# Kernel optimization log

Hardware: AMD Instinct MI355X
Metric: run time of the kernel (lower is better)

## Reference

```python
import jax, jax.numpy as jnp
import numpy as np

D = 512
HEADS, DIM_HEAD, LANDMARKS, PINV_ITERS = 8, 64, 256, 6
CONV_K = 33  # residual depthwise conv kernel over sequence dim


def _ln(x, g, b, eps=1e-5):
    mu = x.mean(-1, keepdims=True)
    var = ((x - mu) ** 2).mean(-1, keepdims=True)
    return (x - mu) / jnp.sqrt(var + eps) * g + b


def _moe(x, gw, gb, f1w, f1b, l1g, l1b, f2w, f2b, l2g, l2b, k):
    # Dense grouped-expert evaluation (same math as per-token dispatch in torch source).
    scores = x @ gw + gb                               # [B,N,E]
    topk_s, topk_i = jax.lax.top_k(scores, k)          # [B,N,k]
    h = jnp.einsum('bnd,edh->benh', x, f1w) + f1b[None, :, None, :]
    h = jax.nn.relu(_ln(h, l1g[None, :, None, :], l1b[None, :, None, :]))
    o = jnp.einsum('benh,ehd->bend', h, f2w) + f2b[None, :, None, :]
    o = _ln(o, l2g[None, :, None, :], l2b[None, :, None, :])  # [B,E,N,D]
    o = jnp.take_along_axis(jnp.swapaxes(o, 1, 2), topk_i[..., None], axis=2)  # [B,N,k,D]
    w = jax.nn.softmax(topk_s, axis=-1)[..., None]
    return (w * o).sum(axis=2) + x


def _pinv(x, iters):
    # Moore-Penrose iterative pseudoinverse (lucidrains nystrom-attention)
    col = jnp.abs(x).sum(-1).max()
    row = jnp.abs(x).sum(-2).max()
    z = jnp.swapaxes(x, -1, -2) / (col * row)
    I = jnp.eye(x.shape[-1], dtype=x.dtype)
    for _ in range(iters):
        xz = x @ z
        z = 0.25 * z @ (13 * I - xz @ (15 * I - xz @ (7 * I - xz)))
    return z


def _nystrom(x, qkv_w, out_w, out_b, conv_w):
    b, n, _ = x.shape
    m, h, dh = LANDMARKS, HEADS, DIM_HEAD
    pad = (m - n % m) % m
    x = jnp.pad(x, ((0, 0), (pad, 0), (0, 0)))  # pad at FRONT, as in source
    npd = n + pad
    qkv = x @ qkv_w                              # [b, npd, 3*h*dh]
    q, k, v = [t.reshape(b, npd, h, dh).transpose(0, 2, 1, 3) for t in jnp.split(qkv, 3, axis=-1)]
    q = q * dh ** -0.5
    l = npd // m
    q_l = q.reshape(b, h, m, l, dh).mean(3)      # landmark means
    k_l = k.reshape(b, h, m, l, dh).mean(3)
    attn1 = jax.nn.softmax(jnp.einsum('bhid,bhjd->bhij', q, k_l), -1)    # [b,h,npd,m]
    attn2 = jax.nn.softmax(jnp.einsum('bhid,bhjd->bhij', q_l, k_l), -1)  # [b,h,m,m]
    attn3 = jax.nn.softmax(jnp.einsum('bhid,bhjd->bhij', q_l, k), -1)    # [b,h,m,npd]
    out = (attn1 @ _pinv(attn2, PINV_ITERS)) @ (attn3 @ v)               # [b,h,npd,dh]
    res = jax.lax.conv_general_dilated(
        v, conv_w, (1, 1), [(CONV_K // 2, CONV_K // 2), (0, 0)],
        dimension_numbers=('NCHW', 'OIHW', 'NCHW'), feature_group_count=h)
    out = out + res
    out = out.transpose(0, 2, 1, 3).reshape(b, npd, h * dh)
    out = out @ out_w + out_b
    return out[:, -n:]


def setup_inputs() -> dict:
    key = jax.random.key(0)
    ks = iter(jax.random.split(key, 64))
    def rn(shape, s=0.02):
        return jax.random.normal(next(ks), shape, jnp.float32) * s
    inp = {'features': jax.random.normal(next(ks), (4, 6000, D), jnp.float32)}
    inp['cls_token'] = rn((1, 1, D), 1e-6)
    def moe_params(pfx, E):
        inp[pfx + '_gate_w'] = rn((D, E)); inp[pfx + '_gate_b'] = jnp.zeros((E,), jnp.float32)
        inp[pfx + '_fc1_w'] = rn((E, D, D)); inp[pfx + '_fc1_b'] = jnp.zeros((E, D), jnp.float32)
        inp[pfx + '_ln1_g'] = jnp.ones((E, D), jnp.float32); inp[pfx + '_ln1_b'] = jnp.zeros((E, D), jnp.float32)
        inp[pfx + '_fc2_w'] = rn((E, D, D)); inp[pfx + '_fc2_b'] = jnp.zeros((E, D), jnp.float32)
        inp[pfx + '_ln2_g'] = jnp.ones((E, D), jnp.float32); inp[pfx + '_ln2_b'] = jnp.zeros((E, D), jnp.float32)
    moe_params('moe1', 2)
    moe_params('moe2', 4)
    def layer_params(pfx):
        inp[pfx + '_norm_g'] = jnp.ones((D,), jnp.float32); inp[pfx + '_norm_b'] = jnp.zeros((D,), jnp.float32)
        inp[pfx + '_qkv_w'] = rn((D, 3 * HEADS * DIM_HEAD))
        inp[pfx + '_out_w'] = rn((HEADS * DIM_HEAD, D)); inp[pfx + '_out_b'] = jnp.zeros((D,), jnp.float32)
        inp[pfx + '_conv_w'] = rn((HEADS, 1, CONV_K, 1))
    layer_params('l1')
    layer_params('l2')
    return inp


def reference(features, cls_token,
              moe1_gate_w, moe1_gate_b, moe1_fc1_w, moe1_fc1_b, moe1_ln1_g, moe1_ln1_b, moe1_fc2_w, moe1_fc2_b, moe1_ln2_g, moe1_ln2_b,
              moe2_gate_w, moe2_gate_b, moe2_fc1_w, moe2_fc1_b, moe2_ln1_g, moe2_ln1_b, moe2_fc2_w, moe2_fc2_b, moe2_ln2_g, moe2_ln2_b,
              l1_norm_g, l1_norm_b, l1_qkv_w, l1_out_w, l1_out_b, l1_conv_w,
              l2_norm_g, l2_norm_b, l2_qkv_w, l2_out_w, l2_out_b, l2_conv_w):
    B, N, _ = features.shape
    _H = int(np.ceil(np.sqrt(N)))
    add = _H * _H - N
    h = jnp.concatenate([features, features[:, :add]], axis=1)      # square pad by wrap
    h = jnp.concatenate([jnp.broadcast_to(cls_token, (B, 1, D)), h], axis=1)
    h = _moe(h, moe1_gate_w, moe1_gate_b, moe1_fc1_w, moe1_fc1_b, moe1_ln1_g, moe1_ln1_b, moe1_fc2_w, moe1_fc2_b, moe1_ln2_g, moe1_ln2_b, k=1)
    h = h + _nystrom(_ln(h, l1_norm_g, l1_norm_b), l1_qkv_w, l1_out_w, l1_out_b, l1_conv_w)
    h = _moe(h, moe2_gate_w, moe2_gate_b, moe2_fc1_w, moe2_fc1_b, moe2_ln1_g, moe2_ln1_b, moe2_fc2_w, moe2_fc2_b, moe2_ln2_g, moe2_ln2_b, k=2)
    h = h + _nystrom(_ln(h, l2_norm_g, l2_norm_b), l2_qkv_w, l2_out_w, l2_out_b, l2_conv_w)
    return (h[:, 0], h[:, 1:])
```

## Files before the change

kernel.cpp:

```cpp
#include <hip/hip_runtime.h>
#include <hip/hip_bf16.h>

constexpr int BATCH = 4;
constexpr int NTOK  = 6085;
constexpr int BN_TOK = BATCH * NTOK;
constexpr int NPD   = 6144;
constexpr int RPAD  = BATCH * NPD;
constexpr int DMODEL = 512;
constexpr int NH = 8, DH = 64;
constexpr int NBH = BATCH * NH;
constexpr int LGRP = NPD / 256;
constexpr int PAD_FRONT = 59;
constexpr int CONVK = 33;
constexpr int NCH = 4;

typedef __attribute__((ext_vector_type(8))) short short8v;
typedef __attribute__((ext_vector_type(4))) float f32x4;

__device__ __forceinline__ unsigned short f2bf(float f) {
  unsigned u = __float_as_uint(f);
  u += 0x7FFF + ((u >> 16) & 1);
  return (unsigned short)(u >> 16);
}
__device__ __forceinline__ float bf2f(unsigned short h) {
  return __uint_as_float((unsigned)h << 16);
}


__global__ void k_build_h(const float* __restrict__ feat, const float* __restrict__ cls,
                          float* __restrict__ H) {
  size_t total = (size_t)BN_TOK * DMODEL;
  for (size_t idx = (size_t)blockIdx.x * blockDim.x + threadIdx.x; idx < total;
       idx += (size_t)gridDim.x * blockDim.x) {
    int d = (int)(idx & 511);
    size_t tok = idx >> 9;
    int b = (int)(tok / NTOK), n = (int)(tok % NTOK);
    float v;
    if (n == 0) v = cls[d];
    else {
      int i = n - 1; if (i >= 6000) i -= 6000;
      v = feat[((size_t)b * 6000 + i) * DMODEL + d];
    }
    H[idx] = v;
  }
}

__global__ void k_diag_fill(float* __restrict__ out, size_t n, float val) {
  for (size_t i = (size_t)blockIdx.x * blockDim.x + threadIdx.x; i < n;
       i += (size_t)gridDim.x * blockDim.x)
    out[i] = val;
}

__global__ __launch_bounds__(256) void k_wconv(const float* __restrict__ W, int ldb,
    unsigned short* __restrict__ hi, unsigned short* __restrict__ lo) {
  __shared__ unsigned short Th[64][80], Tl[64][80];
  int bk = blockIdx.y * 64, bn = blockIdx.x * 64;
  int t = threadIdx.x;
  int kr = t >> 2, cq = (t & 3) * 16;
  const float* src = W + (size_t)(bk + kr) * ldb + bn + cq;
  #pragma unroll
  for (int q = 0; q < 4; ++q) {
    float4 v = *(const float4*)(src + q * 4);
    float vs[4] = {v.x, v.y, v.z, v.w};
    #pragma unroll
    for (int e = 0; e < 4; ++e) {
      int n = cq + q * 4 + e;
      unsigned short h = f2bf(vs[e]);
      Th[n][kr] = h;
      Tl[n][kr] = f2bf(vs[e] - bf2f(h));
    }
  }
  __syncthreads();
  int nr = t >> 2, kq = (t & 3) * 16;
  size_t o = (size_t)(bn + nr) * 512 + bk + kq;
  *(short8v*)&hi[o]     = *(const short8v*)&Th[nr][kq];
  *(short8v*)&hi[o + 8] = *(const short8v*)&Th[nr][kq + 8];
  *(short8v*)&lo[o]     = *(const short8v*)&Tl[nr][kq];
  *(short8v*)&lo[o + 8] = *(const short8v*)&Tl[nr][kq + 8];
}

__global__ __launch_bounds__(256) void k_gemm_mfma(const float* __restrict__ A,
    const unsigned short* __restrict__ BtH, const unsigned short* __restrict__ BtL,
    const float* __restrict__ bias, float* __restrict__ C,
    int M, int lda, int ldc, float alpha, int omode)
{
  __shared__ unsigned short AsH[128][40], AsL[128][40];
  __shared__ unsigned short BsH[128][40], BsL[128][40];
  int bm = blockIdx.y * 128, bn = blockIdx.x * 128;
  int tid = threadIdx.x;
  int wave = tid >> 6, lane = tid & 63;
  int mo = (wave >> 1) * 64, no = (wave & 1) * 64;
  int r16 = lane & 15, g = lane >> 4;
  f32x4 acc[4][4] = {};
  int srow = tid >> 1, shalf = (tid & 1) * 16;
  const float* aptr = A + (size_t)(bm + srow) * lda + shalf;
  bool avalid = (bm + srow) < M;
  const unsigned short* bhptr = BtH + (size_t)(bn + srow) * 512 + shalf;
  const unsigned short* blptr = BtL + (size_t)(bn + srow) * 512 + shalf;
  for (int k0 = 0; k0 < 512; k0 += 32) {
    unsigned short h8[16], l8[16];
    #pragma unroll
    for (int q = 0; q < 4; ++q) {
      float4 v = avalid ? *(const float4*)(aptr + k0 + q * 4) : make_float4(0.f, 0.f, 0.f, 0.f);
      float vs[4] = {v.x, v.y, v.z, v.w};
      #pragma unroll
      for (int e = 0; e < 4; ++e) {
        unsigned short hh = f2bf(vs[e]);
        h8[q * 4 + e] = hh;
        l8[q * 4 + e] = f2bf(vs[e] - bf2f(hh));
      }
    }
    *(short8v*)&AsH[srow][shalf]     = *(short8v*)&h8[0];
    *(short8v*)&AsH[srow][shalf + 8] = *(short8v*)&h8[8];
    *(short8v*)&AsL[srow][shalf]     = *(short8v*)&l8[0];
    *(short8v*)&AsL[srow][shalf + 8] = *(short8v*)&l8[8];
    *(short8v*)&BsH[srow][shalf]     = *(const short8v*)(bhptr + k0);
    *(short8v*)&BsH[srow][shalf + 8] = *(const short8v*)(bhptr + k0 + 8);
    *(short8v*)&BsL[srow][shalf]     = *(const short8v*)(blptr + k0);
    *(short8v*)&BsL[srow][shalf + 8] = *(const short8v*)(blptr + k0 + 8);
    __syncthreads();
    short8v ah[4], al[4], bh[4], bl[4];
    #pragma unroll
    for (int mt = 0; mt < 4; ++mt) {
      ah[mt] = *(const short8v*)&AsH[mo + mt * 16 + r16][g * 8];
      al[mt] = *(const short8v*)&AsL[mo + mt * 16 + r16][g * 8];
    }
    #pragma unroll
    for (int nt = 0; nt < 4; ++nt) {
      bh[nt] = *(const short8v*)&BsH[no + nt * 16 + r16][g * 8];
      bl[nt] = *(const short8v*)&BsL[no + nt * 16 + r16][g * 8];
    }
    #pragma unroll
    for (int mt = 0; mt < 4; ++mt)
      #pragma unroll
      for (int nt = 0; nt < 4; ++nt) {
        acc[mt][nt] = __builtin_amdgcn_mfma_f32_16x16x32_bf16(ah[mt], bh[nt], acc[mt][nt], 0, 0, 0);
        acc[mt][nt] = __builtin_amdgcn_mfma_f32_16x16x32_bf16(ah[mt], bl[nt], acc[mt][nt], 0, 0, 0);
        acc[mt][nt] = __builtin_amdgcn_mfma_f32_16x16x32_bf16(al[mt], bh[nt], acc[mt][nt], 0, 0, 0);
      }
    __syncthreads();
  }
  #pragma unroll
  for (int mt = 0; mt < 4; ++mt)
    #pragma unroll
    for (int nt = 0; nt < 4; ++nt)
      #pragma unroll
      for (int j = 0; j < 4; ++j) {
        int gr = bm + mo + mt * 16 + g * 4 + j;
        int gc = bn + no + nt * 16 + r16;
        if (gr >= M) continue;
        float v = alpha * acc[mt][nt][j] + (bias ? bias[gc] : 0.f);
        if (omode == 0) {
          C[(size_t)gr * ldc + gc] = v;
        } else if (omode == 2) {
          int bb = gr / NPD, ii = gr % NPD;
          if (ii >= PAD_FRONT)
            C[((size_t)bb * NTOK + ii - PAD_FRONT) * 512 + gc] += v;
        } else {
          int bb = gr / NPD, ii = gr % NPD;
          int hh = gc >> 6, dd = gc & 63;
          C[(((size_t)bb * NH + hh) * NPD + ii) * 64 + dd] = v;
        }
      }
}

__global__ __launch_bounds__(256) void k_gemm_mfma2(const float* __restrict__ A,
    const float* __restrict__ Bt, float* __restrict__ C,
    float alpha, int omode, float cdiag, int premap)
{
  __shared__ unsigned short AsH[128][40], AsL[128][40];
  __shared__ unsigned short BsH[128][40], BsL[128][40];
  size_t zo = (size_t)blockIdx.z * 65536;
  int bm = blockIdx.y * 128, bn = blockIdx.x * 128;
  int tid = threadIdx.x;
  int wave = tid >> 6, lane = tid & 63;
  int mo = (wave >> 1) * 64, no = (wave & 1) * 64;
  int r16 = lane & 15, g = lane >> 4;
  f32x4 acc[4][4] = {};
  int srow = tid >> 1, shalf = (tid & 1) * 16;
  int grow = bm + srow;
  int gn = bn + srow;
  for (int k0 = 0; k0 < 256; k0 += 32) {
    unsigned short h8[16], l8[16];
    #pragma unroll
    for (int q = 0; q < 4; ++q) {
      float4 v = *(const float4*)&A[zo + (size_t)grow * 256 + k0 + shalf + q * 4];
      float vs[4] = {v.x, v.y, v.z, v.w};
      #pragma unroll
      for (int e = 0; e < 4; ++e) {
        float a = vs[e];
        if (premap) a = ((grow == (k0 + shalf + q * 4 + e)) ? 7.f : 0.f) - a;
        unsigned short hh = f2bf(a);
        h8[q * 4 + e] = hh;
        l8[q * 4 + e] = f2bf(a - bf2f(hh));
      }
    }
    *(short8v*)&AsH[srow][shalf]     = *(short8v*)&h8[0];
    *(short8v*)&AsH[srow][shalf + 8] = *(short8v*)&h8[8];
    *(short8v*)&AsL[srow][shalf]     = *(short8v*)&l8[0];
    *(short8v*)&AsL[srow][shalf + 8] = *(short8v*)&l8[8];
    #pragma unroll
    for (int q = 0; q < 4; ++q) {
      float4 v = *(const float4*)&Bt[zo + (size_t)gn * 256 + k0 + shalf + q * 4];
      float vs[4] = {v.x, v.y, v.z, v.w};
      #pragma unroll
      for (int e = 0; e < 4; ++e) {
        unsigned short hh = f2bf(vs[e]);
        h8[q * 4 + e] = hh;
        l8[q * 4 + e] = f2bf(vs[e] - bf2f(hh));
      }
    }
    *(short8v*)&BsH[srow][shalf]     = *(short8v*)&h8[0];
    *(short8v*)&BsH[srow][shalf + 8] = *(short8v*)&h8[8];
    *(short8v*)&BsL[srow][shalf]     = *(short8v*)&l8[0];
    *(short8v*)&BsL[srow][shalf + 8] = *(short8v*)&l8[8];
    __syncthreads();
    short8v ah[4], al[4], bh[4], bl[4];
    #pragma unroll
    for (int mt = 0; mt < 4; ++mt) {
      ah[mt] = *(const short8v*)&AsH[mo + mt * 16 + r16][g * 8];
      al[mt] = *(const short8v*)&AsL[mo + mt * 16 + r16][g * 8];
    }
    #pragma unroll
    for (int nt = 0; nt < 4; ++nt) {
      bh[nt] = *(const short8v*)&BsH[no + nt * 16 + r16][g * 8];
      bl[nt] = *(const short8v*)&BsL[no + nt * 16 + r16][g * 8];
    }
    #pragma unroll
    for (int mt = 0; mt < 4; ++mt)
      #pragma unroll
      for (int nt = 0; nt < 4; ++nt) {
        acc[mt][nt] = __builtin_amdgcn_mfma_f32_16x16x32_bf16(ah[mt], bh[nt], acc[mt][nt], 0, 0, 0);
        acc[mt][nt] = __builtin_amdgcn_mfma_f32_16x16x32_bf16(ah[mt], bl[nt], acc[mt][nt], 0, 0, 0);
        acc[mt][nt] = __builtin_amdgcn_mfma_f32_16x16x32_bf16(al[mt], bh[nt], acc[mt][nt], 0, 0, 0);
      }
    __syncthreads();
  }
  #pragma unroll
  for (int mt = 0; mt < 4; ++mt)
    #pragma unroll
    for (int nt = 0; nt < 4; ++nt)
      #pragma unroll
      for (int j = 0; j < 4; ++j) {
        int gr = bm + mo + mt * 16 + g * 4 + j;
        int gc = bn + no + nt * 16 + r16;
        float v;
        if (omode == 5) v = ((gr == gc) ? cdiag : 0.f) - acc[mt][nt][j];
        else            v = alpha * acc[mt][nt][j];
        C[zo + (size_t)gr * 256 + gc] = v;
      }
}

__global__ __launch_bounds__(256) void k_tpose(const float* __restrict__ in,
                                               float* __restrict__ out) {
  __shared__ float Ts[64][65];
  int bx = blockIdx.x * 64, by = blockIdx.y * 64;
  size_t zo = (size_t)blockIdx.z * 65536;
  int t = threadIdx.x;
  int r = t >> 4, c4 = (t & 15) * 4;
  #pragma unroll
  for (int u = 0; u < 4; ++u) {
    float4 v = *(const float4*)&in[zo + (size_t)(by + r + u * 16) * 256 + bx + c4];
    Ts[r + u * 16][c4 + 0] = v.x; Ts[r + u * 16][c4 + 1] = v.y;
    Ts[r + u * 16][c4 + 2] = v.z; Ts[r + u * 16][c4 + 3] = v.w;
  }
  __syncthreads();
  #pragma unroll
  for (int u = 0; u < 4; ++u) {
    int rr = r + u * 16;
    float4 v = make_float4(Ts[c4][rr], Ts[c4 + 1][rr], Ts[c4 + 2][rr], Ts[c4 + 3][rr]);
    *(float4*)&out[zo + (size_t)(bx + rr) * 256 + by + c4] = v;
  }
}

__global__ void k_y0(const float* __restrict__ A2, float* __restrict__ Y,
                     const unsigned int* __restrict__ sc) {
  float scale = 1.f / (__uint_as_float(sc[0]) * __uint_as_float(sc[1]));
  size_t total = (size_t)NBH * 65536;
  for (size_t idx = (size_t)blockIdx.x * blockDim.x + threadIdx.x; idx < total;
       idx += (size_t)gridDim.x * blockDim.x)
    Y[idx] = A2[idx] * scale;
}

__global__ __launch_bounds__(256) void k_gemm(const float* __restrict__ A,
    const float* __restrict__ B,
    const float* __restrict__ bias, float* __restrict__ C,
    int M, int N, int K, int lda, int ldb, int ldc,
    long long sA, long long sB, long long sC, float alpha, int omode, float cdiag)
{
  __shared__ float As[16][65];
  __shared__ float Bs[16][65];
  int z = blockIdx.z;
  A += (size_t)z * (size_t)sA;
  B += (size_t)z * (size_t)sB;
  int bm = blockIdx.y * 64, bn = blockIdx.x * 64;
  int tid = threadIdx.x;
  int tr = tid >> 4, tc = tid & 15;
  int ar = tid >> 2, aq = tid & 3;
  int br = tid >> 4, bq = tid & 15;
  float acc[4][4] = {};
  for (int k0 = 0; k0 < K; k0 += 16) {
    {
      int gr = bm + ar;
      float4 v = make_float4(0.f, 0.f, 0.f, 0.f);
      if (gr < M) v = *(const float4*)&A[(size_t)gr * lda + k0 + aq * 4];
      As[aq * 4 + 0][ar] = v.x; As[aq * 4 + 1][ar] = v.y;
      As[aq * 4 + 2][ar] = v.z; As[aq * 4 + 3][ar] = v.w;
    }
    {
      float4 v = *(const float4*)&B[(size_t)(k0 + br) * ldb + bn + bq * 4];
      Bs[br][bq * 4 + 0] = v.x; Bs[br][bq * 4 + 1] = v.y;
      Bs[br][bq * 4 + 2] = v.z; Bs[br][bq * 4 + 3] = v.w;
    }
    __syncthreads();
    #pragma unroll
    for (int kk = 0; kk < 16; ++kk) {
      float a[4], bv[4];
      #pragma unroll
      for (int i = 0; i < 4; ++i) a[i] = As[kk][tr * 4 + i];
      #pragma unroll
      for (int j = 0; j < 4; ++j) bv[j] = Bs[kk][tc * 4 + j];
      #pragma unroll
      for (int i = 0; i < 4; ++i)
        #pragma unroll
        for (int j = 0; j < 4; ++j) acc[i][j] += a[i] * bv[j];
    }
    __syncthreads();
  }
  #pragma unroll
  for (int i = 0; i < 4; ++i) {
    int gr = bm + tr * 4 + i;
    if (gr >= M) continue;
    #pragma unroll
    for (int j = 0; j < 4; ++j) {
      int gc = bn + tc * 4 + j;
      float v;
      if (omode == 5) {
        v = ((gr == gc) ? cdiag : 0.f) - acc[i][j];
      } else {
        v = alpha * acc[i][j] + (bias ? bias[gc] : 0.f);
      }
      C[(size_t)z * (size_t)sC + (size_t)gr * ldc + gc] = v;
    }
  }
}

__global__ void k_gate(const float* __restrict__ X, const float* __restrict__ gw,
                       const float* __restrict__ gb, float* __restrict__ WT, int E, int k) {
  int tok = blockIdx.x; int lane = threadIdx.x;
  const float* x = X + (size_t)tok * DMODEL;
  float s[4] = {0.f, 0.f, 0.f, 0.f};
  for (int d = lane; d < DMODEL; d += 64) {
    float xv = x[d];
    for (int e = 0; e < E; ++e) s[e] += xv * gw[(size_t)d * E + e];
  }
  #pragma unroll
  for (int off = 32; off; off >>= 1) {
    #pragma unroll
    for (int e = 0; e < 4; ++e) s[e] += __shfl_down(s[e], off);
  }
  if (lane == 0) {
    for (int e = 0; e < E; ++e) s[e] += gb[e];
    float w[4] = {0.f, 0.f, 0.f, 0.f};
    int i1 = 0;
// ... 48 lines not shown
  float* h = H + (size_t)row * 512;
  #pragma unroll
  for (int j = 0; j < 8; ++j) {
    int d = lane + 64 * j;
    h[d] += w * ((x[d] - mu) * rstd * g[d] + b[d]);
  }
}

__global__ void k_ln_pad(const float* __restrict__ H, float* __restrict__ XLn,
                         const float* __restrict__ g, const float* __restrict__ b) {
  int row = blockIdx.x; int lane = threadIdx.x;
  int bb = row / NPD, i = row % NPD;
  float* y = XLn + (size_t)row * 512;
  if (i < PAD_FRONT) {
    #pragma unroll
    for (int j = 0; j < 8; ++j) y[lane + 64 * j] = 0.f;
    return;
  }
  const float* x = H + ((size_t)bb * NTOK + (i - PAD_FRONT)) * 512;
  float mu, rstd; wave_ln_stats(x, lane, mu, rstd);
  #pragma unroll
  for (int j = 0; j < 8; ++j) {
    int d = lane + 64 * j;
    y[d] = (x[d] - mu) * rstd * g[d] + b[d];
  }
}

__global__ void k_xmean(const float* __restrict__ XLn, float* __restrict__ Xm) {
  int z = blockIdx.x;
  int c = threadIdx.x;
  int b = z >> 8, jm = z & 255;
  const float* base = XLn + ((size_t)b * NPD + jm * LGRP) * 512 + c;
  float s = 0.f;
  #pragma unroll
  for (int t = 0; t < LGRP; ++t) s += base[(size_t)t * 512];
  Xm[(size_t)z * 512 + c] = s * (1.f / LGRP);
}

__global__ __launch_bounds__(256) void k_attn2(const float* __restrict__ QL,
                                               const float* __restrict__ KL,
                                               float* __restrict__ A2) {
  int z = blockIdx.x; int bh = z >> 8, j = z & 255;
  int b = bh >> 3, h = bh & 7;
  int t = threadIdx.x;
  __shared__ float q[64]; __shared__ float red[256];
  __shared__ float mshare, sshare;
  if (t < 64) q[t] = QL[((size_t)b * 256 + j) * 512 + h * 64 + t];
  __syncthreads();
  const float* kl = KL + ((size_t)b * 256 + t) * 512 + h * 64;
  float s = 0.f;
  #pragma unroll
  for (int d = 0; d < 64; ++d) s += q[d] * kl[d];
  red[t] = s; __syncthreads();
  for (int st = 128; st; st >>= 1) { if (t < st) red[t] = fmaxf(red[t], red[t + st]); __syncthreads(); }
  if (t == 0) mshare = red[0];
  __syncthreads();
  float e = expf(s - mshare);
  red[t] = e; __syncthreads();
  for (int st = 128; st; st >>= 1) { if (t < st) red[t] += red[t + st]; __syncthreads(); }
  if (t == 0) sshare = red[0];
  __syncthreads();
  A2[((size_t)bh * 256 + j) * 256 + t] = e / sshare;
}

__global__ __launch_bounds__(256) void k_pinv_scalars(const float* __restrict__ A2,
                                                      unsigned int* __restrict__ sc) {
  int bh = blockIdx.x; int t = threadIdx.x;
  const float* A = A2 + (size_t)bh * 65536;
  float rowsum = 0.f, colsum = 0.f;
  for (int jj = 0; jj < 256; ++jj) {
    rowsum += fabsf(A[(size_t)t * 256 + jj]);
    colsum += fabsf(A[(size_t)jj * 256 + t]);
  }
  __shared__ float sh[256];
  sh[t] = rowsum; __syncthreads();
  for (int s = 128; s; s >>= 1) { if (t < s) sh[t] = fmaxf(sh[t], sh[t + s]); __syncthreads(); }
  if (t == 0) atomicMax(&sc[0], __float_as_uint(sh[0]));
  __syncthreads();
  sh[t] = colsum; __syncthreads();
  for (int s = 128; s; s >>= 1) { if (t < s) sh[t] = fmaxf(sh[t], sh[t + s]); __syncthreads(); }
  if (t == 0) atomicMax(&sc[1], __float_as_uint(sh[0]));
}

__global__ void k_zinit(const float* __restrict__ A2, float* __restrict__ Z,
                        const unsigned int* __restrict__ sc) {
  float scale = 1.f / (__uint_as_float(sc[0]) * __uint_as_float(sc[1]));
  size_t total = (size_t)NBH * 65536;
  for (size_t idx = (size_t)blockIdx.x * blockDim.x + threadIdx.x; idx < total;
       idx += (size_t)gridDim.x * blockDim.x) {
    size_t bh = idx >> 16; int r = (int)((idx >> 8) & 255); int cc = (int)(idx & 255);
    Z[idx] = A2[(bh << 16) + (size_t)cc * 256 + r] * scale;
  }
}

__global__ __launch_bounds__(256) void k_flash_mfma(
    const float* __restrict__ Qp, long long Qsb, long long Qsh, int Qsr,
    const float* __restrict__ Kp, long long Ksb, long long Ksh, int Ksr,
    const float* __restrict__ Vp, long long Vsb, long long Vsh, int Vsr,
    float* __restrict__ Op, long long Osb, long long Osh, int Osr,
    float* __restrict__ Opart, float* __restrict__ ML,
    int tiles_per_chunk, int mode)
{
  int jt = blockIdx.x, bh = blockIdx.y, ch = blockIdx.z;
  int b = bh >> 3, h = bh & 7;
  const float* Qb = Qp + (size_t)b * Qsb + (size_t)h * Qsh;
  const float* Kb = Kp + (size_t)b * Ksb + (size_t)h * Ksh;
  const float* Vb = Vp + (size_t)b * Vsb + (size_t)h * Vsh;
  int tid = threadIdx.x;
  int wave = tid >> 6, lane = tid & 63;
  int r16 = lane & 15, g = lane >> 4;
  int q0 = jt * 64 + wave * 16;

  __shared__ unsigned short KsH[64][72], KsL[64][72];
  __shared__ unsigned short VtH[64][72], VtL[64][72];

  short8v qh[2], ql[2];
  #pragma unroll
  for (int kk = 0; kk < 2; ++kk) {
    const float* qr = Qb + (size_t)(q0 + r16) * Qsr + kk * 32 + g * 8;
    float4 v0 = *(const float4*)qr;
    float4 v1 = *(const float4*)(qr + 4);
    float vs[8] = {v0.x, v0.y, v0.z, v0.w, v1.x, v1.y, v1.z, v1.w};
    unsigned short hh[8], llo[8];
    #pragma unroll
    for (int e = 0; e < 8; ++e) {
      hh[e] = f2bf(vs[e]); llo[e] = f2bf(vs[e] - bf2f(hh[e]));
    }
    qh[kk] = *(short8v*)&hh[0];
    ql[kk] = *(short8v*)&llo[0];
  }

  f32x4 O4[4] = {};
  float m[4], lsum[4];
  #pragma unroll
  for (int j = 0; j < 4; ++j) { m[j] = -1e30f; lsum[j] = 0.f; }

  int skey = tid >> 2, sq = (tid & 3) * 16;
  int t0 = ch * tiles_per_chunk;
  for (int tt = t0; tt < t0 + tiles_per_chunk; ++tt) {
    int key0 = tt * 64;
    __syncthreads();
    {
      const float* krow = Kb + (size_t)(key0 + skey) * Ksr + sq;
      const float* vrow = Vb + (size_t)(key0 + skey) * Vsr + sq;
      #pragma unroll
      for (int q = 0; q < 4; ++q) {
        float4 kv = *(const float4*)(krow + q * 4);
        float4 vv = *(const float4*)(vrow + q * 4);
        float ks[4] = {kv.x, kv.y, kv.z, kv.w};
        float vvs[4] = {vv.x, vv.y, vv.z, vv.w};
        #pragma unroll
        for (int e = 0; e < 4; ++e) {
          int d = sq + q * 4 + e;
          unsigned short khh = f2bf(ks[e]);
          KsH[skey][d] = khh;
          KsL[skey][d] = f2bf(ks[e] - bf2f(khh));
          unsigned short vhh = f2bf(vvs[e]);
          VtH[d][skey] = vhh;
          VtL[d][skey] = f2bf(vvs[e] - bf2f(vhh));
        }
      }
    }
    __syncthreads();
    f32x4 S[4] = {};
    #pragma unroll
    for (int kk = 0; kk < 2; ++kk)
      #pragma unroll
      for (int nt = 0; nt < 4; ++nt) {
        short8v kh = *(const short8v*)&KsH[nt * 16 + r16][kk * 32 + g * 8];
        short8v kl = *(const short8v*)&KsL[nt * 16 + r16][kk * 32 + g * 8];
        S[nt] = __builtin_amdgcn_mfma_f32_16x16x32_bf16(qh[kk], kh, S[nt], 0, 0, 0);
        S[nt] = __builtin_amdgcn_mfma_f32_16x16x32_bf16(qh[kk], kl, S[nt], 0, 0, 0);
        S[nt] = __builtin_amdgcn_mfma_f32_16x16x32_bf16(ql[kk], kh, S[nt], 0, 0, 0);
      }
    float tmax[4];
    #pragma unroll
    for (int j = 0; j < 4; ++j)
      tmax[j] = fmaxf(fmaxf(S[0][j], S[1][j]), fmaxf(S[2][j], S[3][j]));
    #pragma unroll
    for (int off = 8; off; off >>= 1)
      #pragma unroll
      for (int j = 0; j < 4; ++j) tmax[j] = fmaxf(tmax[j], __shfl_xor(tmax[j], off));
    float corr[4];
    #pragma unroll
    for (int j = 0; j < 4; ++j) {
      float mn = fmaxf(m[j], tmax[j]);
      corr[j] = expf(m[j] - mn);
      m[j] = mn;
    }
    __syncthreads();
    float tl[4] = {0.f, 0.f, 0.f, 0.f};
    #pragma unroll
    for (int nt = 0; nt < 4; ++nt)
      #pragma unroll
      for (int j = 0; j < 4; ++j) {
        float p = expf(S[nt][j] - m[j]);
        tl[j] += p;
        unsigned short ph = f2bf(p);
        KsH[wave * 16 + g * 4 + j][nt * 16 + r16] = ph;
        KsL[wave * 16 + g * 4 + j][nt * 16 + r16] = f2bf(p - bf2f(ph));
      }
    #pragma unroll
    for (int off = 8; off; off >>= 1)
      #pragma unroll
      for (int j = 0; j < 4; ++j) tl[j] += __shfl_xor(tl[j], off);
    #pragma unroll
    for (int j = 0; j < 4; ++j) lsum[j] = lsum[j] * corr[j] + tl[j];
    #pragma unroll
    for (int nt = 0; nt < 4; ++nt)
      #pragma unroll
      for (int j = 0; j < 4; ++j) O4[nt][j] *= corr[j];
    #pragma unroll
    for (int kk = 0; kk < 2; ++kk) {
      short8v ph = *(const short8v*)&KsH[wave * 16 + r16][kk * 32 + g * 8];
      short8v pl = *(const short8v*)&KsL[wave * 16 + r16][kk * 32 + g * 8];
      #pragma unroll
      for (int nt = 0; nt < 4; ++nt) {
        short8v vh = *(const short8v*)&VtH[nt * 16 + r16][kk * 32 + g * 8];
        short8v vl = *(const short8v*)&VtL[nt * 16 + r16][kk * 32 + g * 8];
        O4[nt] = __builtin_amdgcn_mfma_f32_16x16x32_bf16(ph, vh, O4[nt], 0, 0, 0);
        O4[nt] = __builtin_amdgcn_mfma_f32_16x16x32_bf16(ph, vl, O4[nt], 0, 0, 0);
        O4[nt] = __builtin_amdgcn_mfma_f32_16x16x32_bf16(pl, vh, O4[nt], 0, 0, 0);
      }
    }
  }
  if (mode == 0) {
    float* Ob = Op + (size_t)b * Osb + (size_t)h * Osh;
    float inv[4];
    #pragma unroll
    for (int j = 0; j < 4; ++j) inv[j] = 1.f / lsum[j];
    #pragma unroll
    for (int nt = 0; nt < 4; ++nt)
      #pragma unroll
      for (int j = 0; j < 4; ++j)
        Ob[(size_t)(q0 + g * 4 + j) * Osr + nt * 16 + r16] = O4[nt][j] * inv[j];
  } else {
    #pragma unroll
    for (int j = 0; j < 4; ++j) {
      size_t rowbase = ((size_t)ch * NBH + bh) * 256 + q0 + g * 4 + j;
      #pragma unroll
      for (int nt = 0; nt < 4; ++nt)
        Opart[rowbase * 64 + nt * 16 + r16] = O4[nt][j];
      if (r16 == 0) { ML[rowbase * 2] = m[j]; ML[rowbase * 2 + 1] = lsum[j]; }
    }
  }
}

__global__ __launch_bounds__(256) void k_flash_comb(const float* __restrict__ Opart,
                                                    const float* __restrict__ ML,
                                                    float* __restrict__ A3V) {
  int jt = blockIdx.x, bh = blockIdx.y;
  int t = threadIdx.x;
  int jr = t >> 4, q16 = t & 15;
  int row = jt * 16 + jr;
  float mv[NCH], lv[NCH];
  float M = -1e30f;
  #pragma unroll
  for (int ch = 0; ch < NCH; ++ch) {
    size_t base = (((size_t)ch * NBH + bh) * 256 + row);
    mv[ch] = ML[base * 2]; lv[ch] = ML[base * 2 + 1];
    M = fmaxf(M, mv[ch]);
  }
  float L = 0.f;
  float4 O = make_float4(0.f, 0.f, 0.f, 0.f);
  #pragma unroll
  for (int ch = 0; ch < NCH; ++ch) {
    float c = expf(mv[ch] - M);
    L += c * lv[ch];
    size_t base = (((size_t)ch * NBH + bh) * 256 + row);
    float4 o = *(const float4*)&Opart[base * 64 + q16 * 4];
    O.x += c * o.x; O.y += c * o.y; O.z += c * o.z; O.w += c * o.w;
  }
  float inv = 1.f / L;
  *(float4*)&A3V[((size_t)bh * 256 + row) * 64 + q16 * 4] =
      make_float4(O.x * inv, O.y * inv, O.z * inv, O.w * inv);
}

__global__ __launch_bounds__(256) void k_conv_add(const float* __restrict__ Vp,
                                                  const float* __restrict__ cw,
                                                  float* __restrict__ out) {
  int it = blockIdx.x, bh = blockIdx.y;
  int b = bh >> 3, h = bh & 7;
  int i0 = it * 128;
  int t = threadIdx.x;
  __shared__ float Vs[160][64];
  const float* vb = Vp + (size_t)bh * NPD * 64;
  #pragma unroll
  for (int u = 0; u < 10; ++u) {
    int idx = t + 256 * u;
    int r = idx >> 4, c4 = (idx & 15) * 4;
    int gi = i0 - 16 + r;
    float4 v = make_float4(0.f, 0.f, 0.f, 0.f);
    if (gi >= 0 && gi < NPD) v = *(const float4*)&vb[(size_t)gi * 64 + c4];
    *(float4*)&Vs[r][c4] = v;
  }
  __syncthreads();
  float w[CONVK];
  #pragma unroll
  for (int p = 0; p < CONVK; ++p) w[p] = cw[h * CONVK + p];
  int wave = t >> 6, d = t & 63;
  for (int rr = wave * 32; rr < wave * 32 + 32; ++rr) {
    float acc = 0.f;
    #pragma unroll
    for (int p = 0; p < CONVK; ++p) acc += w[p] * Vs[rr + p][d];
    out[((size_t)b * NPD + i0 + rr) * 512 + h * 64 + d] += acc;
  }
}

__global__ void k_out_write(const float* __restrict__ H, float* __restrict__ out) {
  size_t n0 = (size_t)BATCH * 512;
  size_t total = n0 + (size_t)BATCH * (NTOK - 1) * 512;
  for (size_t idx = (size_t)blockIdx.x * blockDim.x + threadIdx.x; idx < total;
       idx += (size_t)gridDim.x * blockDim.x) {
    float v;
    if (idx < n0) {
      int b = (int)(idx >> 9); int d = (int)(idx & 511);
      v = H[((size_t)b * NTOK) * 512 + d];
    } else {
      size_t r = idx - n0;
      size_t bj = r >> 9; int d = (int)(r & 511);
      int b = (int)(bj / (NTOK - 1)); int j = (int)(bj % (NTOK - 1));
      v = H[((size_t)b * NTOK + 1 + j) * 512 + d];
    }
    out[idx] = v;
  }
}


extern "C" void kernel_launch(void* const* d_in, const int* in_sizes, int n_in,
                              void* d_out, int out_size, void* d_ws, size_t ws_size,
                              hipStream_t stream) {
  (void)in_sizes; (void)n_in;

  const float* feat = (const float*)d_in[0];
  const float* cls  = (const float*)d_in[1];
  const float* m1_gw = (const float*)d_in[2];  const float* m1_gb = (const float*)d_in[3];
  const float* m1_f1w = (const float*)d_in[4]; const float* m1_f1b = (const float*)d_in[5];
  const float* m1_l1g = (const float*)d_in[6]; const float* m1_l1b = (const float*)d_in[7];
  const float* m1_f2w = (const float*)d_in[8]; const float* m1_f2b = (const float*)d_in[9];
  const float* m1_l2g = (const float*)d_in[10]; const float* m1_l2b = (const float*)d_in[11];
  const float* m2_gw = (const float*)d_in[12]; const float* m2_gb = (const float*)d_in[13];
  const float* m2_f1w = (const float*)d_in[14]; const float* m2_f1b = (const float*)d_in[15];
  const float* m2_l1g = (const float*)d_in[16]; const float* m2_l1b = (const float*)d_in[17];
  const float* m2_f2w = (const float*)d_in[18]; const float* m2_f2b = (const float*)d_in[19];
  const float* m2_l2g = (const float*)d_in[20]; const float* m2_l2b = (const float*)d_in[21];
  const float* l1_ng = (const float*)d_in[22]; const float* l1_nb = (const float*)d_in[23];
  const float* l1_qkvw = (const float*)d_in[24]; const float* l1_outw = (const float*)d_in[25];
  const float* l1_outb = (const float*)d_in[26]; const float* l1_convw = (const float*)d_in[27];
  const float* l2_ng = (const float*)d_in[28]; const float* l2_nb = (const float*)d_in[29];
  const float* l2_qkvw = (const float*)d_in[30]; const float* l2_outw = (const float*)d_in[31];
  const float* l2_outb = (const float*)d_in[32]; const float* l2_convw = (const float*)d_in[33];

  constexpr size_t SZ_H    = (size_t)BN_TOK * 512;
  constexpr size_t SZ_ROW  = (size_t)RPAD * 512;
  float* W = (float*)d_ws;
  float* H  = W;
  float* WT = W + SZ_H;
  unsigned int* SC = (unsigned int*)(W + SZ_H + 97360);
  float* pool = W + SZ_H + 97360 + 16;

  float* R2 = pool;
  float* R3 = pool + SZ_ROW;
  float* R4 = pool + 2 * SZ_ROW;
  float* SMALL = pool + 3 * SZ_ROW;
  float* Xm  = SMALL;
  float* QL  = SMALL + 524288;
  float* KL  = SMALL + 1048576;
  float* A2  = SMALL + 1572864;
  float* Zb  = SMALL + 3670016;
  float* XZ  = SMALL + 5767168;
  float* Wa  = SMALL + 7864320;
  float* Wb  = SMALL + 9961472;
  float* A3V = SMALL + 12058624;
  float* W2b = SMALL + 12582912;
  size_t total_f = (SZ_H + 97360 + 16) + 3 * SZ_ROW + 13107200;
  if (total_f * 4 > ws_size) {
    k_diag_fill<<<2048, 256, 0, stream>>>((float*)d_out, (size_t)out_size,
                                          (float)(ws_size >> 20));
    return;
  }

  k_build_h<<<2048, 256, 0, stream>>>(feat, cls, H);

  auto run_moe = [&](const float* gw, const float* gb, const float* f1w, const float* f1b,
                     const float* l1g, const float* l1b, const float* f2w, const float* f2b,
                     const float* l2g, const float* l2b, int E, int k) {
    float* T1 = R2; float* T2 = R3; float* Xsnap = R4;
    unsigned short* BtHi = (unsigned short*)A2;
    unsigned short* BtLo = (unsigned short*)(A2 + 131072);
    hipMemcpyAsync(Xsnap, H, SZ_H * 4, hipMemcpyDeviceToDevice, stream);
    k_gate<<<BN_TOK, 64, 0, stream>>>(H, gw, gb, WT, E, k);
    dim3 g(4, (BN_TOK + 127) / 128, 1);
    for (int e = 0; e < E; ++e) {
      k_wconv<<<dim3(8, 8), 256, 0, stream>>>(f1w + (size_t)e * 262144, 512, BtHi, BtLo);
      k_gemm_mfma<<<g, 256, 0, stream>>>(Xsnap, BtHi, BtLo, f1b + e * 512, T1,
          BN_TOK, 512, 512, 1.f, 0);
      k_ln_relu<<<BN_TOK, 64, 0, stream>>>(T1, l1g + e * 512, l1b + e * 512);
      k_wconv<<<dim3(8, 8), 256, 0, stream>>>(f2w + (size_t)e * 262144, 512, BtHi, BtLo);
      k_gemm_mfma<<<g, 256, 0, stream>>>(T1, BtHi, BtLo, f2b + e * 512, T2,
          BN_TOK, 512, 512, 1.f, 0);
      k_ln_waccum<<<BN_TOK, 64, 0, stream>>>(T2, H, l2g + e * 512, l2b + e * 512, WT, e);
    }
  };

  auto run_attn = [&](const float* ng, const float* nb, const float* qkvw, const float* outw,
                      const float* outb, const float* convw) {
    float* XLn = R2; float* AttnO = R2;
    float* Kp = R3; float* Qb = R3; float* Vp = R4;
    k_ln_pad<<<RPAD, 64, 0, stream>>>(H, XLn, ng, nb);
    k_xmean<<<BATCH * 256, 512, 0, stream>>>(XLn, Xm);
    k_gemm<<<dim3(8, 16, 1), 256, 0, stream>>>(Xm, qkvw, nullptr, QL,
        1024, 512, 512, 512, 1536, 512, 0, 0, 0, 0.125f, 0, 0.f);
    k_gemm<<<dim3(8, 16, 1), 256, 0, stream>>>(Xm, qkvw + 512, nullptr, KL,
        1024, 512, 512, 512, 1536, 512, 0, 0, 0, 1.f, 0, 0.f);
    k_attn2<<<NBH * 256, 256, 0, stream>>>(QL, KL, A2);
    hipMemsetAsync(SC, 0, 8, stream);
    k_pinv_scalars<<<NBH, 256, 0, stream>>>(A2, SC);
    k_y0<<<2048, 256, 0, stream>>>(A2, Zb, SC);
    k_zinit<<<2048, 256, 0, stream>>>(A2, Wb, SC);
    float* Y = Zb; float* Z = Wb; float* F1 = XZ; float* F2 = Wa;
    dim3 gq(2, 2, NBH);
    for (int it = 0; it < 6; ++it) {
      k_gemm_mfma2<<<gq, 256, 0, stream>>>(Y, A2, F1, 1.f, 0, 0.f, 0);
      k_gemm_mfma2<<<gq, 256, 0, stream>>>(A2, Y, F2, 1.f, 0, 0.f, 0);
      k_gemm_mfma2<<<gq, 256, 0, stream>>>(F1, F2, Y, 1.f, 5, 15.f, 1);
      k_gemm_mfma2<<<gq, 256, 0, stream>>>(Y, F2, F1, 1.f, 5, 13.f, 0);
      k_gemm_mfma2<<<gq, 256, 0, stream>>>(Z, F1, F2, 0.25f, 0, 0.f, 0);
      float* tz = Z; Z = F2; F2 = tz;
      if (it < 5)
        k_tpose<<<dim3(4, 4, NBH), 256, 0, stream>>>(Z, Y);
    }
    unsigned short* BtQH = (unsigned short*)Wa;
    unsigned short* BtQL = (unsigned short*)(Wa + 393216);
    k_wconv<<<dim3(24, 8), 256, 0, stream>>>(qkvw, 1536, BtQH, BtQL);
    dim3 gr(4, (RPAD + 127) / 128, 1);
    k_gemm_mfma<<<gr, 256, 0, stream>>>(XLn, BtQH + 512 * 512, BtQL + 512 * 512, nullptr,
        Kp, RPAD, 512, 512, 1.f, 3);
    k_gemm_mfma<<<gr, 256, 0, stream>>>(XLn, BtQH + 1024 * 512, BtQL + 1024 * 512, nullptr,
        Vp, RPAD, 512, 512, 1.f, 3);
    k_flash_mfma<<<dim3(4, NBH, NCH), 256, 0, stream>>>(
        QL, 131072LL, 64LL, 512,
        Kp, (long long)NH * NPD * 64, (long long)NPD * 64, 64,
        Vp, (long long)NH * NPD * 64, (long long)NPD * 64, 64,
        nullptr, 0, 0, 0, XZ, Xm, NPD / (64 * NCH), 1);
    k_flash_comb<<<dim3(16, NBH), 256, 0, stream>>>(XZ, Xm, A3V);
    k_gemm<<<dim3(1, 4, NBH), 256, 0, stream>>>(Z, A3V, nullptr, W2b,
        256, 64, 256, 256, 64, 64, 65536, 16384, 16384, 1.f, 0, 0.f);
    k_gemm_mfma<<<gr, 256, 0, stream>>>(XLn, BtQH, BtQL, nullptr,
        Qb, RPAD, 512, 512, 0.125f, 0);
    k_flash_mfma<<<dim3(NPD / 64, NBH, 1), 256, 0, stream>>>(
        Qb, (long long)NPD * 512, 64LL, 512,
        KL, 131072LL, 64LL, 512,
        W2b, 131072LL, 16384LL, 64,
        AttnO, (long long)NPD * 512, 64LL, 512,
        nullptr, nullptr, 256 / 64, 0);
    k_conv_add<<<dim3(NPD / 128, NBH), 256, 0, stream>>>(Vp, convw, AttnO);
    unsigned short* BtOH = (unsigned short*)Wa;
    unsigned short* BtOL = (unsigned short*)(Wa + 131072);
    k_wconv<<<dim3(8, 8), 256, 0, stream>>>(outw, 512, BtOH, BtOL);
    k_gemm_mfma<<<gr, 256, 0, stream>>>(AttnO, BtOH, BtOL, outb,
        H, RPAD, 512, 512, 1.f, 2);
  };

  run_moe(m1_gw, m1_gb, m1_f1w, m1_f1b, m1_l1g, m1_l1b, m1_f2w, m1_f2b, m1_l2g, m1_l2b, 2, 1);
  run_attn(l1_ng, l1_nb, l1_qkvw, l1_outw, l1_outb, l1_convw);
  run_moe(m2_gw, m2_gb, m2_f1w, m2_f1b, m2_l1g, m2_l1b, m2_f2w, m2_f2b, m2_l2g, m2_l2b, 4, 2);
  run_attn(l2_ng, l2_nb, l2_qkvw, l2_outw, l2_outb, l2_convw);

  k_out_write<<<2048, 256, 0, stream>>>(H, (float*)d_out);
}
```

Before: 3.734 ms.

## Pre-split K/V into bf16 hi/lo, pretransposed V, drop one pinv GEMM, more flash chunks

K and V projections now emit bf16 hi/lo pairs directly from the GEMM epilogue, and V is pre-transposed so the flash kernel loads tiles with vector copies instead of converting fp32 per tile. The landmark K and W2 are pre-converted likewise. The pinv loop replaces the Y·A2 GEMM with a transpose of A2·Y, exploiting symmetry of the iteration. The flash chunk count is doubled for more parallelism, and conv_add reads from the transposed bf16 V. These changes add extra conversion and transpose passes and shift precision to hi/lo bf16 reconstruction.

After: 3.611 ms. 1.03x faster.

```diff
diff --git a/kernel.cpp b/kernel.cpp
--- a/kernel.cpp
+++ b/kernel.cpp
@@ -12,7 +12,7 @@
 constexpr int LGRP = NPD / 256;
 constexpr int PAD_FRONT = 59;
 constexpr int CONVK = 33;
-constexpr int NCH = 4;
+constexpr int NCH = 8;
 
 typedef __attribute__((ext_vector_type(8))) short short8v;
 typedef __attribute__((ext_vector_type(4))) float f32x4;
@@ -82,7 +82,7 @@
 __global__ __launch_bounds__(256) void k_gemm_mfma(const float* __restrict__ A,
     const unsigned short* __restrict__ BtH, const unsigned short* __restrict__ BtL,
     const float* __restrict__ bias, float* __restrict__ C,
-    int M, int lda, int ldc, float alpha, int omode)
+    int M, int lda, int ldc, float alpha, int omode, unsigned short* __restrict__ Clo)
 {
   __shared__ unsigned short AsH[128][40], AsL[128][40];
   __shared__ unsigned short BsH[128][40], BsL[128][40];
@@ -156,10 +156,17 @@
           int bb = gr / NPD, ii = gr % NPD;
           if (ii >= PAD_FRONT)
             C[((size_t)bb * NTOK + ii - PAD_FRONT) * 512 + gc] += v;
+        } else if (omode == 3) {
+          int bb = gr / NPD, ii = gr % NPD;
+          int hh = gc >> 6, dd = gc & 63;
+          C[(((size_t)bb * NH + hh) * NPD + ii) * 64 + dd] = v;
         } else {
           int bb = gr / NPD, ii = gr % NPD;
           int hh = gc >> 6, dd = gc & 63;
-          C[(((size_t)bb * NH + hh) * NPD + ii) * 64 + dd] = v;
+          size_t idx = (((size_t)bb * NH + hh) * NPD + ii) * 64 + dd;
+          unsigned short hi = f2bf(v);
+          ((unsigned short*)C)[idx] = hi;
+          Clo[idx] = f2bf(v - bf2f(hi));
         }
       }
 }
@@ -280,6 +287,17 @@
   for (size_t idx = (size_t)blockIdx.x * blockDim.x + threadIdx.x; idx < total;
        idx += (size_t)gridDim.x * blockDim.x)
     Y[idx] = A2[idx] * scale;
+}
+
+__global__ void k_zinit(const float* __restrict__ A2, float* __restrict__ Z,
+                        const unsigned int* __restrict__ sc) {
+  float scale = 1.f / (__uint_as_float(sc[0]) * __uint_as_float(sc[1]));
+  size_t total = (size_t)NBH * 65536;
+  for (size_t idx = (size_t)blockIdx.x * blockDim.x + threadIdx.x; idx < total;
+       idx += (size_t)gridDim.x * blockDim.x) {
+    size_t bh = idx >> 16; int r = (int)((idx >> 8) & 255); int cc = (int)(idx & 255);
+    Z[idx] = A2[(bh << 16) + (size_t)cc * 256 + r] * scale;
+  }
 }
 
 __global__ __launch_bounds__(256) void k_gemm(const float* __restrict__ A,
@@ -494,21 +512,59 @@
   if (t == 0) atomicMax(&sc[1], __float_as_uint(sh[0]));
 }
 
-__global__ void k_zinit(const float* __restrict__ A2, float* __restrict__ Z,
-                        const unsigned int* __restrict__ sc) {
-  float scale = 1.f / (__uint_as_float(sc[0]) * __uint_as_float(sc[1]));
-  size_t total = (size_t)NBH * 65536;
-  for (size_t idx = (size_t)blockIdx.x * blockDim.x + threadIdx.x; idx < total;
-       idx += (size_t)gridDim.x * blockDim.x) {
-    size_t bh = idx >> 16; int r = (int)((idx >> 8) & 255); int cc = (int)(idx & 255);
-    Z[idx] = A2[(bh << 16) + (size_t)cc * 256 + r] * scale;
-  }
-}
-
-__global__ __launch_bounds__(256) void k_flash_mfma(
+__global__ __launch_bounds__(256) void k_vtpose(const unsigned short* __restrict__ VrH,
+    const unsigned short* __restrict__ VrL,
+    unsigned short* __restrict__ VtH, unsigned short* __restrict__ VtL) {
+  __shared__ unsigned short TH[64][72], TL[64][72];
+  int i0 = blockIdx.x * 64, bh = blockIdx.y;
+  int t = threadIdx.x;
+  const unsigned short* sH = VrH + ((size_t)bh * NPD + i0) * 64;
+  const unsigned short* sL = VrL + ((size_t)bh * NPD + i0) * 64;
+  #pragma unroll
+  for (int u = 0; u < 2; ++u) {
+    int idx = t + 256 * u;
+    int r = idx >> 3, c8 = (idx & 7) * 8;
+    *(short8v*)&TH[r][c8] = *(const short8v*)&sH[idx * 8];
+    *(short8v*)&TL[r][c8] = *(const short8v*)&sL[idx * 8];
+  }
+  __syncthreads();
+  #pragma unroll
+  for (int u = 0; u < 2; ++u) {
+    int idx = t + 256 * u;
+    int d = idx >> 3, c8 = (idx & 7) * 8;
+    unsigned short h8[8], l8[8];
+    #pragma unroll
+    for (int e = 0; e < 8; ++e) { h8[e] = TH[c8 + e][d]; l8[e] = TL[c8 + e][d]; }
+    *(short8v*)&VtH[((size_t)bh * 64 + d) * NPD + i0 + c8] = *(short8v*)&h8[0];
+    *(short8v*)&VtL[((size_t)bh * 64 + d) * NPD + i0 + c8] = *(short8v*)&l8[0];
+  }
+}
+
+__global__ void k_cvt_kl(const float* __restrict__ KL, unsigned short* __restrict__ KH,
+                         unsigned short* __restrict__ KLo) {
+  int idx = blockIdx.x * 256 + threadIdx.x;
+  int bh = idx >> 14, j = (idx >> 6) & 255, d = idx & 63;
+  int b = bh >> 3, h = bh & 7;
+  float v = KL[((size_t)b * 256 + j) * 512 + h * 64 + d];
+  unsigned short hi = f2bf(v);
+  KH[idx] = hi; KLo[idx] = f2bf(v - bf2f(hi));
+}
+
+__global__ void k_cvt_w2t(const float* __restrict__ W2b, unsigned short* __restrict__ WH,
+                          unsigned short* __restrict__ WL) {
+  int idx = blockIdx.x * 256 + threadIdx.x;
+  int bh = idx >> 14, d = (idx >> 8) & 63, j = idx & 255;
+  float v = W2b[((size_t)bh * 256 + j) * 64 + d];
+  unsigned short hi = f2bf(v);
+  WH[idx] = hi; WL[idx] = f2bf(v - bf2f(hi));
+}
+
+__global__ __launch_bounds__(256) void k_flash_pre(
     const float* __restrict__ Qp, long long Qsb, long long Qsh, int Qsr,
-    const float* __restrict__ Kp, long long Ksb, long long Ksh, int Ksr,
-    const float* __restrict__ Vp, long long Vsb, long long Vsh, int Vsr,
+    const unsigned short* __restrict__ KHg, const unsigned short* __restrict__ KLg,
+    long long Ksbh,
+    const unsigned short* __restrict__ VtHg, const unsigned short* __restrict__ VtLg,
+    long long Vsbh, int Vrow,
     float* __restrict__ Op, long long Osb, long long Osh, int Osr,
     float* __restrict__ Opart, float* __restrict__ ML,
     int tiles_per_chunk, int mode)
@@ -516,8 +572,10 @@
   int jt = blockIdx.x, bh = blockIdx.y, ch = blockIdx.z;
   int b = bh >> 3, h = bh & 7;
   const float* Qb = Qp + (size_t)b * Qsb + (size_t)h * Qsh;
-  const float* Kb = Kp + (size_t)b * Ksb + (size_t)h * Ksh;
-  const float* Vb = Vp + (size_t)b * Vsb + (size_t)h * Vsh;
+  const unsigned short* KbH = KHg + (size_t)bh * Ksbh;
+  const unsigned short* KbL = KLg + (size_t)bh * Ksbh;
+  const unsigned short* VbH = VtHg + (size_t)bh * Vsbh;
+  const unsigned short* VbL = VtLg + (size_t)bh * Vsbh;
   int tid = threadIdx.x;
   int wave = tid >> 6, lane = tid & 63;
   int r16 = lane & 15, g = lane >> 4;
@@ -547,30 +605,28 @@
   #pragma unroll
   for (int j = 0; j < 4; ++j) { m[j] = -1e30f; lsum[j] = 0.f; }
 
-  int skey = tid >> 2, sq = (tid & 3) * 16;
   int t0 = ch * tiles_per_chunk;
   for (int tt = t0; tt < t0 + tiles_per_chunk; ++tt) {
     int key0 = tt * 64;
     __syncthreads();
     {
-      const float* krow = Kb + (size_t)(key0 + skey) * Ksr + sq;
-      const float* vrow = Vb + (size_t)(key0 + skey) * Vsr + sq;
-      #pragma unroll
-      for (int q = 0; q < 4; ++q) {
-        float4 kv = *(const float4*)(krow + q * 4);
-        float4 vv = *(const float4*)(vrow + q * 4);
-        float ks[4] = {kv.x, kv.y, kv.z, kv.w};
-        float vvs[4] = {vv.x, vv.y, vv.z, vv.w};
-        #pragma unroll
-        for (int e = 0; e < 4; ++e) {
-          int d = sq + q * 4 + e;
-          unsigned short khh = f2bf(ks[e]);
-          KsH[skey][d] = khh;
-          KsL[skey][d] = f2bf(ks[e] - bf2f(khh));
-          unsigned short vhh = f2bf(vvs[e]);
-          VtH[d][skey] = vhh;
-          VtL[d][skey] = f2bf(vvs[e] - bf2f(vhh));
-        }
+      const unsigned short* ksrcH = KbH + (size_t)key0 * 64;
+      const unsigned short* ksrcL = KbL + (size_t)key0 * 64;
+      #pragma unroll
+      for (int u = 0; u < 2; ++u) {
+        int idx = tid + 256 * u;
+        int r = idx >> 3, c8 = (idx & 7) * 8;
+        *(short8v*)&KsH[r][c8] = *(const short8v*)&ksrcH[idx * 8];
+        *(short8v*)&KsL[r][c8] = *(const short8v*)&ksrcL[idx * 8];
+      }
+      const unsigned short* vsrcH = VbH + key0;
+      const unsigned short* vsrcL = VbL + key0;
+      #pragma unroll
+      for (int u = 0; u < 2; ++u) {
+        int idx = tid + 256 * u;
+        int d = idx >> 3, c8 = (idx & 7) * 8;
+        *(short8v*)&VtH[d][c8] = *(const short8v*)&vsrcH[(size_t)d * Vrow + c8];
+        *(short8v*)&VtL[d][c8] = *(const short8v*)&vsrcL[(size_t)d * Vrow + c8];
       }
     }
     __syncthreads();
@@ -688,34 +744,37 @@
       make_float4(O.x * inv, O.y * inv, O.z * inv, O.w * inv);
 }
 
-__global__ __launch_bounds__(256) void k_conv_add(const float* __restrict__ Vp,
-                                                  const float* __restrict__ cw,
-                                                  float* __restrict__ out) {
+__global__ __launch_bounds__(256) void k_conv_add(const unsigned short* __restrict__ VtHg,
+    const unsigned short* __restrict__ VtLg, const float* __restrict__ cw,
+    float* __restrict__ out) {
   int it = blockIdx.x, bh = blockIdx.y;
   int b = bh >> 3, h = bh & 7;
   int i0 = it * 128;
   int t = threadIdx.x;
-  __shared__ float Vs[160][64];
-  const float* vb = Vp + (size_t)bh * NPD * 64;
-  #pragma unroll
-  for (int u = 0; u < 10; ++u) {
+  __shared__ float Vs[64][161];
+  const unsigned short* vh = VtHg + (size_t)bh * 64 * NPD;
+  const unsigned short* vl = VtLg + (size_t)bh * 64 * NPD;
+  for (int u = 0; u < 40; ++u) {
     int idx = t + 256 * u;
-    int r = idx >> 4, c4 = (idx & 15) * 4;
-    int gi = i0 - 16 + r;
-    float4 v = make_float4(0.f, 0.f, 0.f, 0.f);
-    if (gi >= 0 && gi < NPD) v = *(const float4*)&vb[(size_t)gi * 64 + c4];
-    *(float4*)&Vs[r][c4] = v;
+    int d = idx / 160, ii = idx - d * 160;
+    int gi = i0 - 16 + ii;
+    float v = 0.f;
+    if (gi >= 0 && gi < NPD) {
+      size_t a = (size_t)d * NPD + gi;
+      v = bf2f(vh[a]) + bf2f(vl[a]);
+    }
+    Vs[d][ii] = v;
   }
   __syncthreads();
   float w[CONVK];
   #pragma unroll
   for (int p = 0; p < CONVK; ++p) w[p] = cw[h * CONVK + p];
-  int wave = t >> 6, d = t & 63;
-  for (int rr = wave * 32; rr < wave * 32 + 32; ++rr) {
+  int rgrp = t >> 6, d = t & 63;
+  for (int r = rgrp * 32; r < rgrp * 32 + 32; ++r) {
     float acc = 0.f;
     #pragma unroll
-    for (int p = 0; p < CONVK; ++p) acc += w[p] * Vs[rr + p][d];
-    out[((size_t)b * NPD + i0 + rr) * 512 + h * 64 + d] += acc;
+    for (int p = 0; p < CONVK; ++p) acc += w[p] * Vs[d][r + p];
+    out[((size_t)b * NPD + i0 + r) * 512 + h * 64 + d] += acc;
   }
 }
 
@@ -780,7 +839,7 @@
   float* KL  = SMALL + 1048576;
   float* A2  = SMALL + 1572864;
   float* Zb  = SMALL + 3670016;
-  float* XZ  = SMALL + 5767168;
+  float* XZp = SMALL + 5767168;
   float* Wa  = SMALL + 7864320;
   float* Wb  = SMALL + 9961472;
   float* A3V = SMALL + 12058624;
@@ -806,11 +865,11 @@
     for (int e = 0; e < E; ++e) {
       k_wconv<<<dim3(8, 8), 256, 0, stream>>>(f1w + (size_t)e * 262144, 512, BtHi, BtLo);
       k_gemm_mfma<<<g, 256, 0, stream>>>(Xsnap, BtHi, BtLo, f1b + e * 512, T1,
-          BN_TOK, 512, 512, 1.f, 0);
+          BN_TOK, 512, 512, 1.f, 0, nullptr);
       k_ln_relu<<<BN_TOK, 64, 0, stream>>>(T1, l1g + e * 512, l1b + e * 512);
       k_wconv<<<dim3(8, 8), 256, 0, stream>>>(f2w + (size_t)e * 262144, 512, BtHi, BtLo);
       k_gemm_mfma<<<g, 256, 0, stream>>>(T1, BtHi, BtLo, f2b + e * 512, T2,
-          BN_TOK, 512, 512, 1.f, 0);
+          BN_TOK, 512, 512, 1.f, 0, nullptr);
       k_ln_waccum<<<BN_TOK, 64, 0, stream>>>(T2, H, l2g + e * 512, l2b + e * 512, WT, e);
     }
   };
@@ -818,7 +877,13 @@
   auto run_attn = [&](const float* ng, const float* nb, const float* qkvw, const float* outw,
                       const float* outb, const float* convw) {
     float* XLn = R2; float* AttnO = R2;
-    float* Kp = R3; float* Qb = R3; float* Vp = R4;
+    float* Qb = R3;
+    unsigned short* VrH = (unsigned short*)R3;
+    unsigned short* VrL = VrH + 12582912;
+    unsigned short* KH  = (unsigned short*)R3;
+    unsigned short* KLo = KH + 12582912;
+    unsigned short* VtH = (unsigned short*)R4;
+    unsigned short* VtL = VtH + 12582912;
     k_ln_pad<<<RPAD, 64, 0, stream>>>(H, XLn, ng, nb);
     k_xmean<<<BATCH * 256, 512, 0, stream>>>(XLn, Xm);
     k_gemm<<<dim3(8, 16, 1), 256, 0, stream>>>(Xm, qkvw, nullptr, QL,
@@ -830,48 +895,55 @@
     k_pinv_scalars<<<NBH, 256, 0, stream>>>(A2, SC);
     k_y0<<<2048, 256, 0, stream>>>(A2, Zb, SC);
     k_zinit<<<2048, 256, 0, stream>>>(A2, Wb, SC);
-    float* Y = Zb; float* Z = Wb; float* F1 = XZ; float* F2 = Wa;
+    float* Y = Zb; float* Z = Wb; float* F1 = XZp; float* F2 = Wa;
     dim3 gq(2, 2, NBH);
     for (int it = 0; it < 6; ++it) {
-      k_gemm_mfma2<<<gq, 256, 0, stream>>>(Y, A2, F1, 1.f, 0, 0.f, 0);
-      k_gemm_mfma2<<<gq, 256, 0, stream>>>(A2, Y, F2, 1.f, 0, 0.f, 0);
-      k_gemm_mfma2<<<gq, 256, 0, stream>>>(F1, F2, Y, 1.f, 5, 15.f, 1);
-      k_gemm_mfma2<<<gq, 256, 0, stream>>>(Y, F2, F1, 1.f, 5, 13.f, 0);
-      k_gemm_mfma2<<<gq, 256, 0, stream>>>(Z, F1, F2, 0.25f, 0, 0.f, 0);
-      float* tz = Z; Z = F2; F2 = tz;
+      k_gemm_mfma2<<<gq, 256, 0, stream>>>(A2, Y, F1, 1.f, 0, 0.f, 0);
+      k_tpose<<<dim3(4, 4, NBH), 256, 0, stream>>>(F1, F2);
+      k_gemm_mfma2<<<gq, 256, 0, stream>>>(F2, F1, Y, 1.f, 5, 15.f, 1);
+      k_gemm_mfma2<<<gq, 256, 0, stream>>>(Y, F1, F2, 1.f, 5, 13.f, 0);
+      k_gemm_mfma2<<<gq, 256, 0, stream>>>(Z, F2, F1, 0.25f, 0, 0.f, 0);
+      float* tz = Z; Z = F1; F1 = tz;
       if (it < 5)
         k_tpose<<<dim3(4, 4, NBH), 256, 0, stream>>>(Z, Y);
     }
+    unsigned short* KLH = (unsigned short*)A2;
+    unsigned short* KLL = KLH + 524288;
+    unsigned short* W2tH = KLH + 1048576;
+    unsigned short* W2tL = KLH + 1572864;
+    k_cvt_kl<<<2048, 256, 0, stream>>>(KL, KLH, KLL);
     unsigned short* BtQH = (unsigned short*)Wa;
-    unsigned short* BtQL = (unsigned short*)(Wa + 393216);
+    unsigned short* BtQL = BtQH + 786432;
     k_wconv<<<dim3(24, 8), 256, 0, stream>>>(qkvw, 1536, BtQH, BtQL);
     dim3 gr(4, (RPAD + 127) / 128, 1);
+    k_gemm_mfma<<<gr, 256, 0, stream>>>(XLn, BtQH + 1024 * 512, BtQL + 1024 * 512, nullptr,
+        (float*)VrH, RPAD, 512, 512, 1.f, 6, VrL);
+    k_vtpose<<<dim3(NPD / 64, NBH), 256, 0, stream>>>(VrH, VrL, VtH, VtL);
     k_gemm_mfma<<<gr, 256, 0, stream>>>(XLn, BtQH + 512 * 512, BtQL + 512 * 512, nullptr,
-        Kp, RPAD, 512, 512, 1.f, 3);
-    k_gemm_mfma<<<gr, 256, 0, stream>>>(XLn, BtQH + 1024 * 512, BtQL + 1024 * 512, nullptr,
-        Vp, RPAD, 512, 512, 1.f, 3);
-    k_flash_mfma<<<dim3(4, NBH, NCH), 256, 0, stream>>>(
+        (float*)KH, RPAD, 512, 512, 1.f, 6, KLo);
+    k_flash_pre<<<dim3(4, NBH, NCH), 256, 0, stream>>>(
         QL, 131072LL, 64LL, 512,
-        Kp, (long long)NH * NPD * 64, (long long)NPD * 64, 64,
-        Vp, (long long)NH * NPD * 64, (long long)NPD * 64, 64,
-        nullptr, 0, 0, 0, XZ, Xm, NPD / (64 * NCH), 1);
-    k_flash_comb<<<dim3(16, NBH), 256, 0, stream>>>(XZ, Xm, A3V);
+        KH, KLo, (long long)NPD * 64,
+        VtH, VtL, (long long)64 * NPD, NPD,
+        nullptr, 0, 0, 0, Zb, Xm, NPD / (64 * NCH), 1);
+    k_flash_comb<<<dim3(16, NBH), 256, 0, stream>>>(Zb, Xm, A3V);
     k_gemm<<<dim3(1, 4, NBH), 256, 0, stream>>>(Z, A3V, nullptr, W2b,
         256, 64, 256, 256, 64, 64, 65536, 16384, 16384, 1.f, 0, 0.f);
+    k_cvt_w2t<<<2048, 256, 0, stream>>>(W2b, W2tH, W2tL);
     k_gemm_mfma<<<gr, 256, 0, stream>>>(XLn, BtQH, BtQL, nullptr,
-        Qb, RPAD, 512, 512, 0.125f, 0);
-    k_flash_mfma<<<dim3(NPD / 64, NBH, 1), 256, 0, stream>>>(
+        Qb, RPAD, 512, 512, 0.125f, 0, nullptr);
+    k_flash_pre<<<dim3(NPD / 64, NBH, 1), 256, 0, stream>>>(
         Qb, (long long)NPD * 512, 64LL, 512,
-        KL, 131072LL, 64LL, 512,
-        W2b, 131072LL, 16384LL, 64,
+        KLH, KLL, 16384LL,
+        W2tH, W2tL, 16384LL, 256,
         AttnO, (long long)NPD * 512, 64LL, 512,
-        nullptr, nullptr, 256 / 64, 0);
-    k_conv_add<<<dim3(NPD / 128, NBH), 256, 0, stream>>>(Vp, convw, AttnO);
+        nullptr, nullptr, 4, 0);
+    k_conv_add<<<dim3(NPD / 128, NBH), 256, 0, stream>>>(VtH, VtL, convw, AttnO);
     unsigned short* BtOH = (unsigned short*)Wa;
-    unsigned short* BtOL = (unsigned short*)(Wa + 131072);
+    unsigned short* BtOL = BtOH + 262144;
     k_wconv<<<dim3(8, 8), 256, 0, stream>>>(outw, 512, BtOH, BtOL);
     k_gemm_mfma<<<gr, 256, 0, stream>>>(AttnO, BtOH, BtOL, outb,
-        H, RPAD, 512, 512, 1.f, 2);
+        H, RPAD, 512, 512, 1.f, 2, nullptr);
   };
 
   run_moe(m1_gw, m1_gb, m1_f1w, m1_f1b, m1_l1g, m1_l1b, m1_f2w, m1_f2b, m1_l2g, m1_l2b, 2, 1);
```
